# Kernel tuning notes

Measured on AMD Instinct MI355X. Metric: run time of the kernel, lower is better.

## Reference

```python
import jax, jax.numpy as jnp
import numpy as np

B, T, C, H = 4, 4096, 1024, 16


def setup_inputs() -> dict:
    key = jax.random.key(0)
    k1, k2, k3 = jax.random.split(key, 3)
    x = jax.random.normal(k1, (B, T, C), dtype=jnp.float32)
    # nn.Linear(d_model, 3*d_model, bias=False): weight shape [3C, C]
    W_qkv = jax.random.normal(k2, (3 * C, C), dtype=jnp.float32) * 0.02
    # output Linear(d_model, d_model): weight [C, C], bias [C]
    W_out = jax.random.normal(k3, (C, C), dtype=jnp.float32) * 0.02
    b_out = jnp.zeros((C,), dtype=jnp.float32)
    return {"x": x, "W_qkv": W_qkv, "W_out": W_out, "b_out": b_out}


def reference(x, W_qkv, W_out, b_out):
    Bs, Ts, Cs = x.shape
    dh = Cs // H
    scale = dh ** (-0.5)
    # qkv projection: [B,T,3C]
    qkv = x @ W_qkv.T
    q, k, v = jnp.split(qkv, 3, axis=-1)

    def to_heads(t):  # [B,T,C] -> [B,H,T,dh]
        return t.reshape(Bs, Ts, H, dh).transpose(0, 2, 1, 3)

    q, k, v = to_heads(q), to_heads(k), to_heads(v)
    # rfft over the sequence dim -> [B,H,F,dh], F = T//2+1 (complex64)
    q_f = jnp.fft.rfft(q, axis=-2)
    k_f = jnp.fft.rfft(k, axis=-2)
    # spectral score: sum over head_dim of conj(q)*k, real part -> [B,H,F]
    attn = jnp.sum(jnp.conj(q_f) * k_f, axis=-1).real * scale
    attn = jax.nn.softmax(attn, axis=-1)  # softmax over frequency bins
    v_f = jnp.fft.rfft(v, axis=-2)
    out = jnp.fft.irfft(attn[..., None] * v_f, n=Ts, axis=-2)  # [B,H,T,dh]
    out = out.transpose(0, 2, 1, 3).reshape(Bs, Ts, Cs)
    # output projection (dropout is identity in eval)
    return out @ W_out.T + b_out
```

## Files before the change

kernel.cpp:

```cpp
#include <hip/hip_runtime.h>
#include <math.h>

#define Bsz   4
#define Tsz   4096
#define Csz   1024
#define Hn    16
#define DHn   64
#define NTOT  (Bsz * Tsz)
#define M3    (3 * Csz)
#define Fn    2049
#define BHn   (Bsz * Hn)
#define HALFN 8192

typedef __bf16 bf16x8 __attribute__((ext_vector_type(8)));
typedef __bf16 bf16x4 __attribute__((ext_vector_type(4)));
typedef float  f32x4  __attribute__((ext_vector_type(4)));

__device__ __forceinline__ void gload_lds16(const void* g, void* l) {
  __builtin_amdgcn_global_load_lds(
      (const __attribute__((address_space(1))) void*)g,
      (__attribute__((address_space(3))) void*)l, 16, 0, 0);
}

__global__ __launch_bounds__(256)
void cvt_hilo_kernel(const float4* __restrict__ in, bf16x4* __restrict__ hi,
                     bf16x4* __restrict__ lo, int n4) {
  int i = blockIdx.x * blockDim.x + threadIdx.x;
  if (i >= n4) return;
  float4 v = in[i];
  bf16x4 h, l;
  h[0] = (__bf16)v.x; h[1] = (__bf16)v.y; h[2] = (__bf16)v.z; h[3] = (__bf16)v.w;
  l[0] = (__bf16)(v.x - (float)h[0]);
  l[1] = (__bf16)(v.y - (float)h[1]);
  l[2] = (__bf16)(v.z - (float)h[2]);
  l[3] = (__bf16)(v.w - (float)h[3]);
  hi[i] = h;
  lo[i] = l;
}

__global__ __launch_bounds__(256)
void transpose_cvt_kernel(const float* __restrict__ src,
                          __bf16* __restrict__ hi, __bf16* __restrict__ lo) {
  __shared__ float tile[64][65];
  const int tid = threadIdx.x;
  const int n0 = blockIdx.x * 64;
  const int c0 = blockIdx.y * 64;
  const int col = tid & 63;
  const int row4 = tid >> 6;
#pragma unroll
  for (int i = 0; i < 16; ++i) {
    const int r = i * 4 + row4;
    tile[r][col] = src[(size_t)(c0 + r) * NTOT + n0 + col];
  }
  __syncthreads();
#pragma unroll
  for (int i = 0; i < 16; ++i) {
    const int n = i * 4 + row4;
    const float v = tile[col][n];
    const __bf16 h = (__bf16)v;
    const __bf16 l = (__bf16)(v - (float)h);
    hi[(size_t)(n0 + n) * Csz + c0 + col] = h;
    lo[(size_t)(n0 + n) * Csz + c0 + col] = l;
  }
}

template<int COLMAP>
__global__ __launch_bounds__(512, 2)
void gemm_8s(const __bf16* __restrict__ Ahi, const __bf16* __restrict__ Alo,
             const __bf16* __restrict__ Bhi, const __bf16* __restrict__ Blo,
             float* __restrict__ C, int ldC, int nbase,
             const float* __restrict__ bias) {
  __shared__ __align__(16) char lds[131072];

  const int tid  = threadIdx.x;
  const int wid  = tid >> 6;
  const int lane = tid & 63;
  const int wm = wid >> 2, wn = wid & 3;

  int bx = blockIdx.x, by = blockIdx.y;
  {
    const int gx = gridDim.x, gy = gridDim.y;
    const int nwg = gx * gy;
    if ((nwg & 7) == 0) {
      const int flat  = by * gx + bx;
      const int chunk = nwg >> 3;
      const int nf    = (flat & 7) * chunk + (flat >> 3);
      if (COLMAP) { bx = nf / gy; by = nf % gy; }
      else        { bx = nf % gx; by = nf / gx; }
    }
  }
  const int m0 = by * 256;
  const int n0 = bx * 256;

  const int r16 = lane & 15;
  const int kc  = lane >> 4;

  const int aq = (wid & 3) + ((wid & 4) ? 4 : 0);
  const int bq = ((wid & 3) << 1) + (wid >> 2);
  const __bf16* gAh = Ahi + (size_t)(m0 + (wid & 3) * 16 + ((wid & 4) ? 128 : 0) + r16) * Csz + kc * 8;
  const __bf16* gAl = Alo + (size_t)(m0 + (wid & 3) * 16 + ((wid & 4) ? 128 : 0) + r16) * Csz + kc * 8;
  const __bf16* gBh = Bhi + (size_t)(n0 + (wid & 3) * 64 + (wid >> 2) * 16 + r16) * Csz + kc * 8;
  const __bf16* gBl = Blo + (size_t)(n0 + (wid & 3) * 64 + (wid >> 2) * 16 + r16) * Csz + kc * 8;

  auto stA = [&](int h, int ts, char* slot) {
    const size_t o = (size_t)h * 64 * Csz + ts * 32;
    gload_lds16(gAh + o, slot + aq * 1024);
    gload_lds16(gAl + o, slot + 8192 + aq * 1024);
  };
  auto stB = [&](int h, int ts, char* slot) {
    const size_t o = (size_t)h * 32 * Csz + ts * 32;
    gload_lds16(gBh + o, slot + bq * 1024);
    gload_lds16(gBl + o, slot + 8192 + bq * 1024);
  };

  f32x4 acc[8][4];
#pragma unroll
  for (int i = 0; i < 8; ++i)
#pragma unroll
    for (int j = 0; j < 4; ++j) acc[i][j] = (f32x4)(0.f);

  stA(0, 0, lds);            stB(0, 0, lds + 16384);
  stB(1, 0, lds + 32768);    stA(1, 0, lds + 49152);
  stA(0, 1, lds + 65536);    stB(0, 1, lds + 81920);

#pragma unroll 1
  for (int t = 0; t < 32; ++t) {
    char* cur = lds + ((t & 1) << 16);
    char* nxt = lds + (((t & 1) ^ 1) << 16);
    bf16x8 ah[4], al[4], bh[4], bl[4];

    if (t < 31) asm volatile("s_waitcnt vmcnt(8)" ::: "memory");
    else        asm volatile("s_waitcnt vmcnt(4)" ::: "memory");
    __builtin_amdgcn_s_barrier();
#pragma unroll
    for (int f = 0; f < 4; ++f) {
      const int off = (wm * 4 + f) * 1024 + lane * 16;
      ah[f] = *(const bf16x8*)(cur + off);
      al[f] = *(const bf16x8*)(cur + 8192 + off);
    }
#pragma unroll
    for (int j = 0; j < 2; ++j) {
      const int off = ((wn << 1) + j) * 1024 + lane * 16;
      bh[j] = *(const bf16x8*)(cur + 16384 + off);
      bl[j] = *(const bf16x8*)(cur + 16384 + 8192 + off);
    }
    if (t < 31) stB(1, t + 1, nxt + 32768);
    asm volatile("s_waitcnt lgkmcnt(0)" ::: "memory");
    __builtin_amdgcn_sched_barrier(0);
    __builtin_amdgcn_s_setprio(1);
#pragma unroll
    for (int f = 0; f < 4; ++f)
#pragma unroll
      for (int j = 0; j < 2; ++j) {
        f32x4 a_ = acc[f][j];
        a_ = __builtin_amdgcn_mfma_f32_16x16x32_bf16(ah[f], bh[j], a_, 0, 0, 0);
        a_ = __builtin_amdgcn_mfma_f32_16x16x32_bf16(ah[f], bl[j], a_, 0, 0, 0);
        a_ = __builtin_amdgcn_mfma_f32_16x16x32_bf16(al[f], bh[j], a_, 0, 0, 0);
        acc[f][j] = a_;
      }
    __builtin_amdgcn_s_setprio(0);

    if (t < 31) asm volatile("s_waitcnt vmcnt(8)" ::: "memory");
    else        asm volatile("s_waitcnt vmcnt(2)" ::: "memory");
    __builtin_amdgcn_s_barrier();
#pragma unroll
    for (int j = 0; j < 2; ++j) {
      const int off = ((wn << 1) + j) * 1024 + lane * 16;
      bh[2 + j] = *(const bf16x8*)(cur + 32768 + off);
      bl[2 + j] = *(const bf16x8*)(cur + 32768 + 8192 + off);
    }
    if (t < 31) stA(1, t + 1, nxt + 49152);
    asm volatile("s_waitcnt lgkmcnt(0)" ::: "memory");
    __builtin_amdgcn_sched_barrier(0);
    __builtin_amdgcn_s_setprio(1);
#pragma unroll
    for (int f = 0; f < 4; ++f)
#pragma unroll
      for (int j = 0; j < 2; ++j) {
        f32x4 a_ = acc[f][2 + j];
        a_ = __builtin_amdgcn_mfma_f32_16x16x32_bf16(ah[f], bh[2 + j], a_, 0, 0, 0);
        a_ = __builtin_amdgcn_mfma_f32_16x16x32_bf16(ah[f], bl[2 + j], a_, 0, 0, 0);
        a_ = __builtin_amdgcn_mfma_f32_16x16x32_bf16(al[f], bh[2 + j], a_, 0, 0, 0);
        acc[f][2 + j] = a_;
      }
    __builtin_amdgcn_s_setprio(0);

    if (t < 31) asm volatile("s_waitcnt vmcnt(8)" ::: "memory");
    else        asm volatile("s_waitcnt vmcnt(0)" ::: "memory");
    __builtin_amdgcn_s_barrier();
#pragma unroll
    for (int f = 0; f < 4; ++f) {
      const int off = (wm * 4 + f) * 1024 + lane * 16;
      ah[f] = *(const bf16x8*)(cur + 49152 + off);
      al[f] = *(const bf16x8*)(cur + 49152 + 8192 + off);
    }
    if (t < 30) stA(0, t + 2, cur);
    asm volatile("s_waitcnt lgkmcnt(0)" ::: "memory");
    __builtin_amdgcn_sched_barrier(0);
    __builtin_amdgcn_s_setprio(1);
#pragma unroll
    for (int f = 0; f < 4; ++f)
#pragma unroll
      for (int j = 0; j < 2; ++j) {
        f32x4 a_ = acc[4 + f][j];
        a_ = __builtin_amdgcn_mfma_f32_16x16x32_bf16(ah[f], bh[j], a_, 0, 0, 0);
        a_ = __builtin_amdgcn_mfma_f32_16x16x32_bf16(ah[f], bl[j], a_, 0, 0, 0);
        a_ = __builtin_amdgcn_mfma_f32_16x16x32_bf16(al[f], bh[j], a_, 0, 0, 0);
        acc[4 + f][j] = a_;
      }
    __builtin_amdgcn_s_setprio(0);

    __builtin_amdgcn_s_barrier();
    if (t < 30) stB(0, t + 2, cur + 16384);
    __builtin_amdgcn_s_setprio(1);
#pragma unroll
    for (int f = 0; f < 4; ++f)
#pragma unroll
      for (int j = 0; j < 2; ++j) {
        f32x4 a_ = acc[4 + f][2 + j];
        a_ = __builtin_amdgcn_mfma_f32_16x16x32_bf16(ah[f], bh[2 + j], a_, 0, 0, 0);
        a_ = __builtin_amdgcn_mfma_f32_16x16x32_bf16(ah[f], bl[2 + j], a_, 0, 0, 0);
        a_ = __builtin_amdgcn_mfma_f32_16x16x32_bf16(al[f], bh[2 + j], a_, 0, 0, 0);
        acc[4 + f][2 + j] = a_;
      }
    __builtin_amdgcn_s_setprio(0);
  }

  const int cm = m0 + wm * 128 + (lane >> 4) * 4;
  const int cn = nbase + n0 + wn * 64 + (lane & 15);
  float bb[4];
#pragma unroll
  for (int g = 0; g < 4; ++g) bb[g] = bias ? bias[cn - nbase + g * 16] : 0.f;
#pragma unroll
  for (int fm = 0; fm < 8; ++fm)
#pragma unroll
    for (int r = 0; r < 4; ++r) {
      float* cp = C + (size_t)(cm + fm * 16 + r) * ldC + cn;
#pragma unroll
      for (int g = 0; g < 4; ++g) cp[g * 16] = acc[fm][g][r] + bb[g];
    }
}

template<int MF>
__global__ __launch_bounds__(512, 2)
void gemm_8p(const __bf16* __restrict__ Ahi, const __bf16* __restrict__ Alo,
             const __bf16* __restrict__ Bhi, const __bf16* __restrict__ Blo,
             float* __restrict__ C, int ldC, int nbase,
             const float* __restrict__ bias, int colmap) {
  constexpr int BM  = 32 * MF;
  constexpr int SA  = BM * 64;
  constexpr int SB  = 16384;
  constexpr int BUF = 2 * SA + 2 * SB;
  __shared__ __align__(16) char lds[2 * BUF];

  const int tid  = threadIdx.x;
  const int wid  = tid >> 6;
  const int lane = tid & 63;
  const int wm = wid >> 2, wn = wid & 3;

  int bx = blockIdx.x, by = blockIdx.y;
  {
    const int gx = gridDim.x, gy = gridDim.y;
    const int nwg = gx * gy;
    if ((nwg & 7) == 0) {
      const int flat  = by * gx + bx;
      const int chunk = nwg >> 3;
      const int nf    = (flat & 7) * chunk + (flat >> 3);
      if (colmap) { bx = nf / gy; by = nf % gy; }
      else        { bx = nf % gx; by = nf / gx; }
    }
  }
  const int m0 = by * BM;
  const int n0 = bx * 256;

  const int r16 = lane & 15;
  const int kc  = lane >> 4;

  const __bf16* gAh0 = Ahi + (size_t)(m0 + wid * 16 + r16) * Csz + kc * 8;
  const __bf16* gAl0 = Alo + (size_t)(m0 + wid * 16 + r16) * Csz + kc * 8;
  const __bf16* gBh0 = Bhi + (size_t)(n0 + wid * 16 + r16) * Csz + kc * 8;
  const __bf16* gBl0 = Blo + (size_t)(n0 + wid * 16 + r16) * Csz + kc * 8;
  const __bf16* gBh1 = gBh0 + (size_t)128 * Csz;
  const __bf16* gBl1 = gBl0 + (size_t)128 * Csz;
  const int dW = wid * 1024;

  f32x4 acc[MF][4];
#pragma unroll
  for (int i = 0; i < MF; ++i)
#pragma unroll
    for (int j = 0; j < 4; ++j) acc[i][j] = (f32x4)(0.f);

  auto stage = [&](char* base, int k0) {
    gload_lds16(gAh0 + k0, base + dW);
    gload_lds16(gAl0 + k0, base + SA + dW);
    gload_lds16(gBh0 + k0, base + 2 * SA + dW);
    gload_lds16(gBh1 + k0, base + 2 * SA + dW + 8192);
    gload_lds16(gBl0 + k0, base + 2 * SA + SB + dW);
    gload_lds16(gBl1 + k0, base + 2 * SA + SB + dW + 8192);
  };

  stage(lds, 0);

  for (int t = 0; t < 32; ++t) {
    char* buf = lds + (t & 1) * BUF;
    asm volatile("s_waitcnt vmcnt(0)" ::: "memory");
    __builtin_amdgcn_s_barrier();
    if (t < 31) stage(lds + ((t & 1) ^ 1) * BUF, (t + 1) * 32);

#pragma unroll
    for (int mh = 0; mh < 2; ++mh) {
      bf16x8 ah[MF / 2], al[MF / 2];
#pragma unroll
      for (int f = 0; f < MF / 2; ++f) {
        const int off = (wm * MF + mh * (MF / 2) + f) * 1024 + lane * 16;
        ah[f] = *(const bf16x8*)(buf + off);
        al[f] = *(const bf16x8*)(buf + SA + off);
      }
#pragma unroll
      for (int nh = 0; nh < 2; ++nh) {
        bf16x8 bh[2], bl[2];
#pragma unroll
        for (int g = 0; g < 2; ++g) {
          const int off = (wn * 4 + nh * 2 + g) * 1024 + lane * 16;
          bh[g] = *(const bf16x8*)(buf + 2 * SA + off);
          bl[g] = *(const bf16x8*)(buf + 2 * SA + SB + off);
        }
        asm volatile("s_waitcnt lgkmcnt(0)" ::: "memory");
        __builtin_amdgcn_sched_barrier(0);
        __builtin_amdgcn_s_setprio(1);
#pragma unroll
        for (int f = 0; f < MF / 2; ++f)
#pragma unroll
          for (int g = 0; g < 2; ++g) {
            f32x4 a_ = acc[mh * (MF / 2) + f][nh * 2 + g];
            a_ = __builtin_amdgcn_mfma_f32_16x16x32_bf16(ah[f], bh[g], a_, 0, 0, 0);
            a_ = __builtin_amdgcn_mfma_f32_16x16x32_bf16(ah[f], bl[g], a_, 0, 0, 0);
            a_ = __builtin_amdgcn_mfma_f32_16x16x32_bf16(al[f], bh[g], a_, 0, 0, 0);
            acc[mh * (MF / 2) + f][nh * 2 + g] = a_;
          }
        __builtin_amdgcn_s_setprio(0);
        __builtin_amdgcn_s_barrier();
      }
    }
  }

  const int cm = m0 + wm * (MF * 16) + (lane >> 4) * 4;
  const int cn = nbase + n0 + wn * 64 + (lane & 15);
  float bb[4];
#pragma unroll
  for (int g = 0; g < 4; ++g) bb[g] = bias ? bias[cn - nbase + g * 16] : 0.f;
#pragma unroll
  for (int fm = 0; fm < MF; ++fm)
#pragma unroll
    for (int r = 0; r < 4; ++r) {
      float* cp = C + (size_t)(cm + fm * 16 + r) * ldC + cn;
#pragma unroll
      for (int g = 0; g < 4; ++g) cp[g * 16] = acc[fm][g][r] + bb[g];
    }
}

__device__ __forceinline__ void fft4096(float2* X, float2* Y, int tid, float sign) {
  float2* src = X;
  float2* dst = Y;
#pragma unroll 1
  for (int stage = 0; stage < 12; ++stage) {
    const int s = 1 << stage;
    __syncthreads();
#pragma unroll
    for (int it = 0; it < 8; ++it) {
      const int idx = tid + (it << 8);
      const int sp = idx & ~(s - 1);
      float2 a = src[idx];
      float2 b = src[idx + 2048];
      float ang = sign * (6.28318530717958647692f / 4096.0f) * (float)sp;
      float sn, cs;
      __sincosf(ang, &sn, &cs);
      float2 sum = make_float2(a.x + b.x, a.y + b.y);
      float2 dif = make_float2(a.x - b.x, a.y - b.y);
      float2 tw  = make_float2(dif.x * cs - dif.y * sn, dif.x * sn + dif.y * cs);
      const int o = idx + sp;
      dst[o] = sum;
      dst[o + s] = tw;
    }
    float2* t = src; src = dst; dst = t;
  }
  __syncthreads();
}

__global__ __launch_bounds__(256)
void qk_cross_kernel(const float* __restrict__ qkT, float* __restrict__ attn_raw,
                     int bhbase) {
  __shared__ float2 bufA[4096];
  __shared__ float2 bufB[4096];
  const int tid = threadIdx.x;
  const int blk = blockIdx.x;
  const int d = blk & 63;
  const int bh = bhbase + (blk >> 6);
  const int h = bh & 15;
  const int b = bh >> 4;

  const float* qrow = qkT + (size_t)(h * DHn + d) * NTOT + b * Tsz;
  const float* krow = qkT + (size_t)(Csz + h * DHn + d) * NTOT + b * Tsz;

  for (int t = tid; t < 4096; t += 256)
    bufA[t] = make_float2(qrow[t], krow[t]);

  fft4096(bufA, bufB, tid, -1.0f);

  float* outp = attn_raw + (size_t)bh * Fn;
  for (int f = tid; f < Fn; f += 256) {
    float2 zf = bufA[f];
    float2 zn = bufA[(4096 - f) & 4095];
    float ar = zf.x + zn.x;
    float ai = zf.y - zn.y;
    float br = zf.x - zn.x;
    float bi = zf.y + zn.y;
    float val = 0.03125f * (ar * bi - ai * br);
    atomicAdd(&outp[f], val);
  }
}

__global__ __launch_bounds__(256)
void softmax_kernel(const float* __restrict__ raw, float* __restrict__ attn) {
  __shared__ float red[256];
  const int tid = threadIdx.x;
  const float* in = raw + (size_t)blockIdx.x * Fn;
  float* outp = attn + (size_t)blockIdx.x * Fn;

  float lmax = -3.4e38f;
  for (int f = tid; f < Fn; f += 256) lmax = fmaxf(lmax, in[f]);
  red[tid] = lmax;
  __syncthreads();
  for (int off = 128; off > 0; off >>= 1) {
    if (tid < off) red[tid] = fmaxf(red[tid], red[tid + off]);
    __syncthreads();
  }
  const float mx = red[0];
  __syncthreads();

  float lsum = 0.f;
  for (int f = tid; f < Fn; f += 256) lsum += __expf(in[f] - mx);
  red[tid] = lsum;
  __syncthreads();
  for (int off = 128; off > 0; off >>= 1) {
    if (tid < off) red[tid] += red[tid + off];
    __syncthreads();
  }
  const float inv = 1.0f / red[0];
  for (int f = tid; f < Fn; f += 256) outp[f] = __expf(in[f] - mx) * inv;
}

__global__ __launch_bounds__(256)
void v_filter_kernel(const float* __restrict__ vT, float* __restrict__ vbarT,
                     const float* __restrict__ attn) {
  __shared__ float2 bufA[4096];
  __shared__ float2 bufB[4096];
  const int tid = threadIdx.x;
  const int blk = blockIdx.x;
  const int jp = blk & 31;
  const int bh = blk >> 5;
  const int h = bh & 15;
  const int b = bh >> 4;
  const int d0 = jp * 2;

  const float* v0 = vT + (size_t)(h * DHn + d0) * NTOT + b * Tsz;
  const float* v1 = v0 + NTOT;

  for (int t = tid; t < 4096; t += 256)
    bufA[t] = make_float2(v0[t], v1[t]);

  fft4096(bufA, bufB, tid, -1.0f);

  const float* a = attn + (size_t)bh * Fn;
  for (int f = tid; f < 4096; f += 256) {
    int fm = (f <= 2048) ? f : (4096 - f);
    float s = a[fm];
    float2 z = bufA[f];
    bufA[f] = make_float2(z.x * s, z.y * s);
  }

  fft4096(bufA, bufB, tid, +1.0f);

  float* y0 = vbarT + (size_t)(h * DHn + d0) * NTOT + b * Tsz;
  float* y1 = y0 + NTOT;
  const float inv = 1.0f / 4096.0f;
  for (int t = tid; t < 4096; t += 256) {
    float2 z = bufA[t];
    y0[t] = z.x * inv;
    y1[t] = z.y * inv;
  }
}

__global__ void zero_kernel(float* __restrict__ p, int n) {
  int i = blockIdx.x * blockDim.x + threadIdx.x;
  if (i < n) p[i] = 0.f;
}

extern "C" void kernel_launch(void* const* d_in, const int* in_sizes, int n_in,
                              void* d_out, int out_size, void* d_ws, size_t ws_size,
                              hipStream_t stream) {
  const float* x    = (const float*)d_in[0];
  const float* Wqkv = (const float*)d_in[1];
  const float* Wout = (const float*)d_in[2];
  const float* bout = (const float*)d_in[3];
  float* out = (float*)d_out;

  char* ws = (char*)d_ws;
  float* qkT      = (float*)ws;
  float* vT       = (float*)ws;
  __bf16* VThi    = (__bf16*)ws;
  __bf16* VTlo    = (__bf16*)(ws + 33554432ull);
  float* vbarT    = (float*)(ws + 67108864ull);
  float* attn_raw = (float*)(ws + 134217728ull);
  float* attn     = (float*)(ws + 134742272ull);
  __bf16* Whi     = (__bf16*)(ws + 135266816ull);
  __bf16* Wlo     = (__bf16*)(ws + 141558272ull);
  __bf16* Xhi     = (__bf16*)(ws + 147849728ull);
  __bf16* Xlo     = (__bf16*)(ws + 164626944ull);
  __bf16* Wouthi  = (__bf16*)(ws + 181404160ull);
  __bf16* Woutlo  = (__bf16*)(ws + 183501312ull);

  const int nraw = BHn * Fn;
  zero_kernel<<<(nraw + 255) / 256, 256, 0, stream>>>(attn_raw, nraw);

  cvt_hilo_kernel<<<3072, 256, 0, stream>>>((const float4*)Wqkv,
                                            (bf16x4*)Whi, (bf16x4*)Wlo, 786432);
  cvt_hilo_kernel<<<1024, 256, 0, stream>>>((const float4*)Wout,
                                            (bf16x4*)Wouthi, (bf16x4*)Woutlo, 262144);

  for (int half = 0; half < 2; ++half) {
    cvt_hilo_kernel<<<8192, 256, 0, stream>>>(
        (const float4*)(x + (size_t)half * HALFN * Csz),
        (bf16x4*)Xhi, (bf16x4*)Xlo, 2097152);
    gemm_8s<1><<<dim3(32, 8), 512, 0, stream>>>(Whi, Wlo, Xhi, Xlo,
                                                qkT, NTOT, half * HALFN, nullptr);
    qk_cross_kernel<<<2048, 256, 0, stream>>>(qkT, attn_raw, half * 32);
    gemm_8p<4><<<dim3(32, 8), 512, 0, stream>>>(Whi + 2048 * Csz, Wlo + 2048 * Csz,
                                                Xhi, Xlo, vT, NTOT, half * HALFN,
                                                nullptr, 1);
  }

  softmax_kernel<<<BHn, 256, 0, stream>>>(attn_raw, attn);

  v_filter_kernel<<<2048, 256, 0, stream>>>(vT, vbarT, attn);

  transpose_cvt_kernel<<<dim3(NTOT / 64, Csz / 64), 256, 0, stream>>>(vbarT, VThi, VTlo);

  gemm_8s<0><<<dim3(4, 64), 512, 0, stream>>>(VThi, VTlo, Wouthi, Woutlo,
                                              out, Csz, 0, bout);
}
```

Before: 653.1 us.

## Switch FFT to radix-4 Stockham with shared-memory twiddle table and vector loads

Replaces the 12-stage radix-2 FFT with a 6-stage radix-4 Stockham FFT, which halves the number of barriers and the number of shared-memory passes. Per-butterfly sincos calls are replaced by a precomputed twiddle table in LDS, with w2 and w3 derived by complex multiplies. Global loads of the q/k and v rows now use float4. This adds 8KB of LDS per block, which may reduce occupancy, and the radix-4 strided LDS accesses may cause bank conflicts.

```diff
diff --git a/kernel.cpp b/kernel.cpp
--- a/kernel.cpp
+++ b/kernel.cpp
@@ -359,28 +359,55 @@
     }
 }
 
-__device__ __forceinline__ void fft4096(float2* X, float2* Y, int tid, float sign) {
+__device__ __forceinline__ void build_twiddle(float2* tw, int tid) {
+  const float k = 6.28318530717958647692f / 4096.0f;
+#pragma unroll
+  for (int i = 0; i < 4; ++i) {
+    const int e = tid + (i << 8);
+    float sn, cs;
+    __sincosf(k * (float)e, &sn, &cs);
+    tw[e] = make_float2(cs, sn);
+  }
+}
+
+__device__ __forceinline__ float2 cmul(float2 a, float2 b) {
+  return make_float2(a.x * b.x - a.y * b.y, a.x * b.y + a.y * b.x);
+}
+
+__device__ __forceinline__ void fft4096_r4(float2* X, float2* Y,
+                                           const float2* __restrict__ tw,
+                                           int tid, float sign) {
   float2* src = X;
   float2* dst = Y;
 #pragma unroll 1
-  for (int stage = 0; stage < 12; ++stage) {
-    const int s = 1 << stage;
+  for (int stage = 0; stage < 6; ++stage) {
+    const int s = 1 << (2 * stage);
     __syncthreads();
 #pragma unroll
-    for (int it = 0; it < 8; ++it) {
+    for (int it = 0; it < 4; ++it) {
       const int idx = tid + (it << 8);
       const int sp = idx & ~(s - 1);
-      float2 a = src[idx];
-      float2 b = src[idx + 2048];
-      float ang = sign * (6.28318530717958647692f / 4096.0f) * (float)sp;
-      float sn, cs;
-      __sincosf(ang, &sn, &cs);
-      float2 sum = make_float2(a.x + b.x, a.y + b.y);
-      float2 dif = make_float2(a.x - b.x, a.y - b.y);
-      float2 tw  = make_float2(dif.x * cs - dif.y * sn, dif.x * sn + dif.y * cs);
-      const int o = idx + sp;
-      dst[o] = sum;
-      dst[o + s] = tw;
+      float2 a0 = src[idx];
+      float2 a1 = src[idx + 1024];
+      float2 a2 = src[idx + 2048];
+      float2 a3 = src[idx + 3072];
+      float2 b0 = make_float2(a0.x + a2.x, a0.y + a2.y);
+      float2 b1 = make_float2(a0.x - a2.x, a0.y - a2.y);
+      float2 b2 = make_float2(a1.x + a3.x, a1.y + a3.y);
+      float2 b3 = make_float2(a1.x - a3.x, a1.y - a3.y);
+      float2 y0 = make_float2(b0.x + b2.x, b0.y + b2.y);
+      float2 y2 = make_float2(b0.x - b2.x, b0.y - b2.y);
+      float2 y1 = make_float2(b1.x - sign * b3.y, b1.y + sign * b3.x);
+      float2 y3 = make_float2(b1.x + sign * b3.y, b1.y - sign * b3.x);
+      float2 w1 = tw[sp];
+      w1.y *= sign;
+      float2 w2 = make_float2(w1.x * w1.x - w1.y * w1.y, 2.f * w1.x * w1.y);
+      float2 w3 = cmul(w1, w2);
+      const int o = idx + 3 * sp;
+      dst[o]         = y0;
+      dst[o + s]     = cmul(w1, y1);
+      dst[o + 2 * s] = cmul(w2, y2);
+      dst[o + 3 * s] = cmul(w3, y3);
     }
     float2* t = src; src = dst; dst = t;
   }
@@ -392,6 +419,7 @@
                      int bhbase) {
   __shared__ float2 bufA[4096];
   __shared__ float2 bufB[4096];
+  __shared__ float2 twid[1024];
   const int tid = threadIdx.x;
   const int blk = blockIdx.x;
   const int d = blk & 63;
@@ -399,13 +427,22 @@
   const int h = bh & 15;
   const int b = bh >> 4;
 
-  const float* qrow = qkT + (size_t)(h * DHn + d) * NTOT + b * Tsz;
-  const float* krow = qkT + (size_t)(Csz + h * DHn + d) * NTOT + b * Tsz;
-
-  for (int t = tid; t < 4096; t += 256)
-    bufA[t] = make_float2(qrow[t], krow[t]);
-
-  fft4096(bufA, bufB, tid, -1.0f);
+  build_twiddle(twid, tid);
+
+  const float4* qrow = (const float4*)(qkT + (size_t)(h * DHn + d) * NTOT + b * Tsz);
+  const float4* krow = (const float4*)(qkT + (size_t)(Csz + h * DHn + d) * NTOT + b * Tsz);
+#pragma unroll
+  for (int i = 0; i < 4; ++i) {
+    const int t4 = tid + (i << 8);
+    float4 qv = qrow[t4];
+    float4 kv = krow[t4];
+    bufA[t4 * 4 + 0] = make_float2(qv.x, kv.x);
+    bufA[t4 * 4 + 1] = make_float2(qv.y, kv.y);
+    bufA[t4 * 4 + 2] = make_float2(qv.z, kv.z);
+    bufA[t4 * 4 + 3] = make_float2(qv.w, kv.w);
+  }
+
+  fft4096_r4(bufA, bufB, twid, tid, -1.0f);
 
   float* outp = attn_raw + (size_t)bh * Fn;
   for (int f = tid; f < Fn; f += 256) {
@@ -455,6 +492,7 @@
                      const float* __restrict__ attn) {
   __shared__ float2 bufA[4096];
   __shared__ float2 bufB[4096];
+  __shared__ float2 twid[1024];
   const int tid = threadIdx.x;
   const int blk = blockIdx.x;
   const int jp = blk & 31;
@@ -463,13 +501,22 @@
   const int b = bh >> 4;
   const int d0 = jp * 2;
 
-  const float* v0 = vT + (size_t)(h * DHn + d0) * NTOT + b * Tsz;
-  const float* v1 = v0 + NTOT;
-
-  for (int t = tid; t < 4096; t += 256)
-    bufA[t] = make_float2(v0[t], v1[t]);
-
-  fft4096(bufA, bufB, tid, -1.0f);
+  build_twiddle(twid, tid);
+
+  const float4* v0 = (const float4*)(vT + (size_t)(h * DHn + d0) * NTOT + b * Tsz);
+  const float4* v1 = (const float4*)(vT + (size_t)(h * DHn + d0 + 1) * NTOT + b * Tsz);
+#pragma unroll
+  for (int i = 0; i < 4; ++i) {
+    const int t4 = tid + (i << 8);
+    float4 av = v0[t4];
+    float4 bv = v1[t4];
+    bufA[t4 * 4 + 0] = make_float2(av.x, bv.x);
+    bufA[t4 * 4 + 1] = make_float2(av.y, bv.y);
+    bufA[t4 * 4 + 2] = make_float2(av.z, bv.z);
+    bufA[t4 * 4 + 3] = make_float2(av.w, bv.w);
+  }
+
+  fft4096_r4(bufA, bufB, twid, tid, -1.0f);
 
   const float* a = attn + (size_t)bh * Fn;
   for (int f = tid; f < 4096; f += 256) {
@@ -479,7 +526,7 @@
     bufA[f] = make_float2(z.x * s, z.y * s);
   }
 
-  fft4096(bufA, bufB, tid, +1.0f);
+  fft4096_r4(bufA, bufB, twid, tid, +1.0f);
 
   float* y0 = vbarT + (size_t)(h * DHn + d0) * NTOT + b * Tsz;
   float* y1 = y0 + NTOT;
```

New measurement: 587.2 us. -10.1%, faster.
